# Kernel tuning notes

Measured on AMD Instinct MI355X. Metric: run time of the kernel, lower is better.

## Reference

```python
import jax, jax.numpy as jnp
import numpy as np

B, N, T, H = 16, 512, 100, 64

def setup_inputs() -> dict:
    key = jax.random.key(0)
    ks = jax.random.split(key, 9)
    s = 0.1
    return {
        "x": jax.random.normal(ks[0], (B, N, T), dtype=jnp.float32),
        "conv1_w": jax.random.normal(ks[1], (16, 1, 3), dtype=jnp.float32) * s,
        "conv1_b": jax.random.normal(ks[2], (16,), dtype=jnp.float32) * s,
        "conv2_w": jax.random.normal(ks[3], (32, 16, 3), dtype=jnp.float32) * s,
        "conv2_b": jax.random.normal(ks[4], (32,), dtype=jnp.float32) * s,
        "W_ih": jax.random.normal(ks[5], (3 * H, 32), dtype=jnp.float32) * s,
        "W_hh": jax.random.normal(ks[6], (3 * H, H), dtype=jnp.float32) * s,
        "b_ih": jax.random.normal(ks[7], (3 * H,), dtype=jnp.float32) * s,
        "b_hh": jax.random.normal(ks[8], (3 * H,), dtype=jnp.float32) * s,
    }

def _causal_conv_relu(h, w, b):
    # h: [BN, C_in, T]; left-pad (k-1)*dilation = 2 for causality
    y = jax.lax.conv_general_dilated(
        h, w, window_strides=(1,), padding=[(2, 0)],
        dimension_numbers=("NCH", "OIH", "NCH"))
    return jax.nn.relu(y + b[None, :, None])

def reference(x, conv1_w, conv1_b, conv2_w, conv2_b, W_ih, W_hh, b_ih, b_hh):
    b_, n_, t_ = x.shape
    h = x.reshape(b_ * n_, 1, t_)
    h = _causal_conv_relu(h, conv1_w, conv1_b)   # [BN, 16, T]
    h = _causal_conv_relu(h, conv2_w, conv2_b)   # [BN, 32, T]
    seq = h.transpose(0, 2, 1)                   # [BN, T, 32]
    # precompute input-to-gate projections for all timesteps: [BN, T, 3H]
    xp = jnp.einsum("btc,gc->btg", seq, W_ih) + b_ih
    hdim = W_hh.shape[1]

    def step(hprev, xt):
        gh = hprev @ W_hh.T + b_hh               # [BN, 3H]
        xr, xz, xn = jnp.split(xt, 3, axis=-1)
        hr, hz, hn = jnp.split(gh, 3, axis=-1)
        r = jax.nn.sigmoid(xr + hr)
        z = jax.nn.sigmoid(xz + hz)
        nn_ = jnp.tanh(xn + r * hn)
        hnew = (1.0 - z) * nn_ + z * hprev
        return hnew, None

    h0 = jnp.zeros((b_ * n_, hdim), dtype=x.dtype)
    hf, _ = jax.lax.scan(step, h0, xp.transpose(1, 0, 2))  # scan over T
    return hf.reshape(b_, n_, hdim)
```

## Files before the change

kernel.cpp:

```cpp
#include <hip/hip_runtime.h>
#include <stdint.h>

typedef __attribute__((ext_vector_type(8))) short s16x8;
typedef __attribute__((ext_vector_type(4))) float f32x4;

__device__ __forceinline__ short f2bf(float f){
  union { float f; uint32_t u; } v; v.f = f;
  uint32_t u = v.u;
  u += 0x7fffu + ((u >> 16) & 1u);
  return (short)(u >> 16);
}
__device__ __forceinline__ float sigm_fast(float x){
  float e = __builtin_amdgcn_exp2f(x * -1.44269504f);
  return __builtin_amdgcn_rcpf(1.f + e);
}
__device__ __forceinline__ float tanh_fast(float x){
  float e = __builtin_amdgcn_exp2f(x * 2.88539008f);
  return __builtin_fmaf(-2.f, __builtin_amdgcn_rcpf(e + 1.f), 1.f);
}

#define MFMA16(a, b, c) __builtin_amdgcn_mfma_f32_16x16x32_bf16((a), (b), (c), 0, 0, 0)

__global__ __launch_bounds__(256, 2) void te_fused(
    const float* __restrict__ x,
    const float* __restrict__ w1, const float* __restrict__ b1,
    const float* __restrict__ w2, const float* __restrict__ b2,
    const float* __restrict__ Wih, const float* __restrict__ Whh,
    const float* __restrict__ bih, const float* __restrict__ bhh,
    float* __restrict__ out)
{
  constexpr int T = 100;
  constexpr int M = 16;
  __shared__ float x_s[M * T];
  __shared__ short hA[2][16 * 72];
  __shared__ short ring[4][16 * 24];
  __shared__ short s_s[2][16 * 40];

  const int tid  = threadIdx.x;
  const int lane = tid & 63;
  const int wv   = tid >> 6;
  const int l15  = lane & 15;
  const int lg   = lane >> 4;
  const int seq0 = blockIdx.x * M;

  {
    const float4* gx = reinterpret_cast<const float4*>(x + (size_t)seq0 * T);
    float4* sx = reinterpret_cast<float4*>(x_s);
    for (int i = tid; i < (M * T) / 4; i += 256) sx[i] = gx[i];
  }
  {
    int* p = reinterpret_cast<int*>(&hA[0][0]);
    for (int i = tid; i < (16 * 72) / 2; i += 256) p[i] = 0;
    int* q = reinterpret_cast<int*>(&ring[0][0]);
    for (int i = tid; i < (4 * 16 * 24) / 2; i += 256) q[i] = 0;
  }

  s16x8 WhhHi[3][2], WihHi[3];
  f32x4 bias_r, bias_z, bias_xn, bias_hn;
#pragma unroll
  for (int g = 0; g < 3; ++g) {
    const int n = 64 * g + 16 * wv + l15;
#pragma unroll
    for (int ks = 0; ks < 2; ++ks) {
      const float* p = Whh + n * 64 + ks * 32 + lg * 8;
#pragma unroll
      for (int j = 0; j < 8; ++j) WhhHi[g][ks][j] = f2bf(p[j]);
    }
    const float* q = Wih + n * 32 + lg * 8;
#pragma unroll
    for (int j = 0; j < 8; ++j) WihHi[g][j] = f2bf(q[j]);
    float bi = bih[n], bh = bhh[n];
    if (g == 0) { float v = bi + bh; bias_r  = (f32x4){v, v, v, v}; }
    if (g == 1) { float v = bi + bh; bias_z  = (f32x4){v, v, v, v}; }
    if (g == 2) { bias_xn = (f32x4){bi, bi, bi, bi};
                  bias_hn = (f32x4){bh, bh, bh, bh}; }
  }

  s16x8 cW2[2];
  f32x4 b2v4;
  {
    const int ch = 16 * (wv & 1) + l15;
    float bv = b2[ch];
    b2v4 = (f32x4){bv, bv, bv, bv};
#pragma unroll
    for (int ks = 0; ks < 2; ++ks) {
      s16x8 h8;
#pragma unroll
      for (int j = 0; j < 8; ++j) {
        const int k = ks * 32 + lg * 8 + j;
        const int g = k >> 4, ii = k & 15;
        h8[j] = (g < 3) ? f2bf(w2[ch * 48 + ii * 3 + g]) : (short)0;
      }
      cW2[ks] = h8;
    }
  }

  const int cidx = tid & 127;
  const int csl  = cidx >> 4;
  const int cch  = cidx & 15;
  const float w1v0 = w1[cch * 3 + 0], w1v1 = w1[cch * 3 + 1], w1v2 = w1[cch * 3 + 2];
  const float b1v = b1[cch];

  const int i0a = (lg & 1) * 8;
  const int grp = lg >> 1;
  const short* ringRdBase = &ring[0][0] + l15 * 24 + i0a;
  int sA0off[4], sA1off[4];
#pragma unroll
  for (int p = 0; p < 4; ++p) {
    sA0off[p] = ((p + 3 + grp) & 3) * 384;
    sA1off[p] = ((p + 1 + grp) & 3) * 384;
  }
  const short* sRdBase = &s_s[0][0] + l15 * 40 + lg * 8;
  const short* hRdBase = &hA[0][0] + l15 * 72 + lg * 8;
  short* hWrBase = &hA[0][0] + (lg * 4) * 72 + 16 * wv + l15;
  short* swWr    = &s_s[0][0] + (lg * 4) * 40 + (wv & 1) * 16 + l15;
  short* ringWrA = &ring[0][0] + csl * 24 + cch;
  short* ringWrB = &ring[0][0] + (csl + 8) * 24 + cch;
  const float* xpA = &x_s[csl * T];
  const float* xpB = &x_s[(csl + 8) * T];

  __syncthreads();

#define CONV2_STEP(P_, WB_) do {                                              \
    s16x8 a0 = *reinterpret_cast<const s16x8*>(ringRdBase + sA0off[(P_)]);    \
    s16x8 a1 = *reinterpret_cast<const s16x8*>(ringRdBase + sA1off[(P_)]);    \
    f32x4 sa = MFMA16(a1, cW2[1], MFMA16(a0, cW2[0], b2v4));                  \
    float m0 = sa[0] > 0.f ? sa[0] : 0.f;                                     \
    float m1 = sa[1] > 0.f ? sa[1] : 0.f;                                     \
    float m2 = sa[2] > 0.f ? sa[2] : 0.f;                                     \
    float m3 = sa[3] > 0.f ? sa[3] : 0.f;                                     \
    uint32_t u01, u23;                                                        \
    asm("v_cvt_pk_bf16_f32 %0, %1, %2" : "=v"(u01) : "v"(m0), "v"(m1));       \
    asm("v_cvt_pk_bf16_f32 %0, %1, %2" : "=v"(u23) : "v"(m2), "v"(m3));       \
    swWr[(WB_) * 640 +   0] = (short)(u01 & 0xffff);                          \
    swWr[(WB_) * 640 +  40] = (short)(u01 >> 16);                             \
    swWr[(WB_) * 640 +  80] = (short)(u23 & 0xffff);                          \
    swWr[(WB_) * 640 + 120] = (short)(u23 >> 16);                             \
  } while (0)

  float xaA = 0.f, xbA = 0.f, xaB = 0.f, xbB = 0.f;
  if (wv >= 2) {
    xaA = xpA[0]; xbA = xpA[1];
    xaB = xpB[0]; xbB = xpB[1];
    float cA = b1v + w1v2 * xaA; cA = cA > 0.f ? cA : 0.f;
    float cB = b1v + w1v2 * xaB; cB = cB > 0.f ? cB : 0.f;
    uint32_t cu;
    asm("v_cvt_pk_bf16_f32 %0, %1, %2" : "=v"(cu) : "v"(cA), "v"(cB));
    ringWrA[0] = (short)(cu & 0xffff);
    ringWrB[0] = (short)(cu >> 16);
  }
  __syncthreads();
  if (wv < 2) CONV2_STEP(3, 0);
  if (wv >= 2) {
    float cA = b1v + w1v1 * xaA + w1v2 * xbA; cA = cA > 0.f ? cA : 0.f;
    float cB = b1v + w1v1 * xaB + w1v2 * xbB; cB = cB > 0.f ? cB : 0.f;
    uint32_t cu;
    asm("v_cvt_pk_bf16_f32 %0, %1, %2" : "=v"(cu) : "v"(cA), "v"(cB));
    ringWrA[384] = (short)(cu & 0xffff);
    ringWrB[384] = (short)(cu >> 16);
  }
  __syncthreads();

  float hreg[4] = {0.f, 0.f, 0.f, 0.f};

#define GRU_STEP(T_, P_, C2_, C1_) do {                                       \
    const int rb_ = (P_) & 1, wb_ = rb_ ^ 1;                                  \
    s16x8 as_ = *reinterpret_cast<const s16x8*>(sRdBase + rb_ * 640);         \
    s16x8 ah0 = *reinterpret_cast<const s16x8*>(hRdBase + rb_ * 1152);        \
    s16x8 ah1 = *reinterpret_cast<const s16x8*>(hRdBase + rb_ * 1152 + 32);   \
    __builtin_amdgcn_s_setprio(1);                                            \
    f32x4 pre_r = MFMA16(as_, WihHi[0],                                       \
                  MFMA16(ah1, WhhHi[0][1],                                    \
                  MFMA16(ah0, WhhHi[0][0], bias_r)));                         \
    f32x4 pre_z = MFMA16(as_, WihHi[1],                                       \
                  MFMA16(ah1, WhhHi[1][1],                                    \
                  MFMA16(ah0, WhhHi[1][0], bias_z)));                         \
    f32x4 xn = MFMA16(as_, WihHi[2], bias_xn);                                \
    f32x4 hn = MFMA16(ah1, WhhHi[2][1],                                       \
               MFMA16(ah0, WhhHi[2][0], bias_hn));                            \
    __builtin_amdgcn_s_setprio(0);                                            \
    if ((C2_) && wv < 2) { CONV2_STEP((P_), wb_); }                           \
    if ((C1_) && wv >= 2) {                                                   \
      float xcA = xpA[(T_) + 2], xcB = xpB[(T_) + 2];                         \
      float cA = b1v + w1v0 * xaA + w1v1 * xbA + w1v2 * xcA;                  \
      cA = cA > 0.f ? cA : 0.f;                                               \
      float cB = b1v + w1v0 * xaB + w1v1 * xbB + w1v2 * xcB;                  \
      cB = cB > 0.f ? cB : 0.f;                                               \
      uint32_t cu_;                                                           \
      asm("v_cvt_pk_bf16_f32 %0, %1, %2" : "=v"(cu_) : "v"(cA), "v"(cB));     \
      ringWrA[(((P_) + 2) & 3) * 384] = (short)(cu_ & 0xffff);                \
      ringWrB[(((P_) + 2) & 3) * 384] = (short)(cu_ >> 16);                   \
      xaA = xbA; xbA = xcA; xaB = xbB; xbB = xcB;                             \
    }                                                                         \
    float hnew[4];                                                            \
    _Pragma("unroll")                                                         \
    for (int i2 = 0; i2 < 4; ++i2) {                                          \
      float r = sigm_fast(pre_r[i2]);                                         \
      float z = sigm_fast(pre_z[i2]);                                         \
      float arg = __builtin_fmaf(r, hn[i2], xn[i2]);                          \
      float tn = tanh_fast(arg);                                              \
      float h = __builtin_fmaf(z, hreg[i2] - tn, tn);                         \
      hreg[i2] = h;                                                           \
      hnew[i2] = h;                                                           \
    }                                                                         \
    uint32_t p01, p23;                                                        \
    asm("v_cvt_pk_bf16_f32 %0, %1, %2" : "=v"(p01) : "v"(hnew[0]), "v"(hnew[1])); \
    asm("v_cvt_pk_bf16_f32 %0, %1, %2" : "=v"(p23) : "v"(hnew[2]), "v"(hnew[3])); \
    hWrBase[wb_ * 1152 +   0] = (short)(p01 & 0xffff);                        \
    hWrBase[wb_ * 1152 +  72] = (short)(p01 >> 16);                           \
    hWrBase[wb_ * 1152 + 144] = (short)(p23 & 0xffff);                        \
    hWrBase[wb_ * 1152 + 216] = (short)(p23 >> 16);                           \
    __syncthreads();                                                          \
  } while (0)

#pragma unroll 1
  for (int t = 0; t < 96; t += 4) {
    GRU_STEP(t + 0, 0, true, true);
    GRU_STEP(t + 1, 1, true, true);
    GRU_STEP(t + 2, 2, true, true);
    GRU_STEP(t + 3, 3, true, true);
  }
  GRU_STEP(96, 0, true, true);
  GRU_STEP(97, 1, true, true);
  GRU_STEP(98, 2, true, false);
  GRU_STEP(99, 3, false, false);

#pragma unroll
  for (int i2 = 0; i2 < 4; ++i2) {
    out[(size_t)(seq0 + lg * 4 + i2) * 64 + 16 * wv + l15] = hreg[i2];
  }
}

extern "C" void kernel_launch(void* const* d_in, const int* in_sizes, int n_in,
                              void* d_out, int out_size, void* d_ws, size_t ws_size,
                              hipStream_t stream)
{
  (void)in_sizes; (void)n_in; (void)d_ws; (void)ws_size; (void)out_size;
  const float* x   = (const float*)d_in[0];
  const float* w1  = (const float*)d_in[1];
  const float* b1  = (const float*)d_in[2];
  const float* w2  = (const float*)d_in[3];
  const float* b2  = (const float*)d_in[4];
  const float* Wih = (const float*)d_in[5];
  const float* Whh = (const float*)d_in[6];
  const float* bih = (const float*)d_in[7];
  const float* bhh = (const float*)d_in[8];
  float* out = (float*)d_out;
  te_fused<<<512, 256, 0, stream>>>(x, w1, b1, w2, b2, Wih, Whh, bih, bhh, out);
}
```

Measured before the change: 74.11 us.

## Process two interleaved 16-sequence GRU chains per block and halve the grid

Each block now handles 32 sequences as two independent 16-row GRU chains, interleaved inside every wave, and the grid drops from 512 to 256 blocks. The MFMA work of the two chains is issued together for instruction-level parallelism, and one barrier per timestep now serves both chains. The conv1 and conv2 producer work is spread across all four waves instead of being split by wave role. Launch bounds drop to one block per CU, which frees registers for the doubled state. The s_setprio hints are removed. This gives up the latency hiding that came from two co-resident blocks per CU, and it raises register and LDS use.

```diff
diff --git a/kernel.cpp b/kernel.cpp
--- a/kernel.cpp
+++ b/kernel.cpp
@@ -21,7 +21,7 @@
 
 #define MFMA16(a, b, c) __builtin_amdgcn_mfma_f32_16x16x32_bf16((a), (b), (c), 0, 0, 0)
 
-__global__ __launch_bounds__(256, 2) void te_fused(
+__global__ __launch_bounds__(256, 1) void te_fused(
     const float* __restrict__ x,
     const float* __restrict__ w1, const float* __restrict__ b1,
     const float* __restrict__ w2, const float* __restrict__ b2,
@@ -30,29 +30,30 @@
     float* __restrict__ out)
 {
   constexpr int T = 100;
-  constexpr int M = 16;
-  __shared__ float x_s[M * T];
-  __shared__ short hA[2][16 * 72];
-  __shared__ short ring[4][16 * 24];
-  __shared__ short s_s[2][16 * 40];
+  __shared__ float x_s[32 * T];
+  __shared__ short hA[2][2][16 * 72];
+  __shared__ short ring[2][4][16 * 24];
+  __shared__ short s_s[2][2][16 * 40];
 
   const int tid  = threadIdx.x;
   const int lane = tid & 63;
   const int wv   = tid >> 6;
   const int l15  = lane & 15;
   const int lg   = lane >> 4;
-  const int seq0 = blockIdx.x * M;
+  const int seq0 = blockIdx.x * 32;
 
   {
     const float4* gx = reinterpret_cast<const float4*>(x + (size_t)seq0 * T);
     float4* sx = reinterpret_cast<float4*>(x_s);
-    for (int i = tid; i < (M * T) / 4; i += 256) sx[i] = gx[i];
-  }
-  {
-    int* p = reinterpret_cast<int*>(&hA[0][0]);
+    for (int i = tid; i < (32 * T) / 4; i += 256) sx[i] = gx[i];
+  }
+  {
+    int* p = reinterpret_cast<int*>(&hA[0][0][0]);
     for (int i = tid; i < (16 * 72) / 2; i += 256) p[i] = 0;
-    int* q = reinterpret_cast<int*>(&ring[0][0]);
-    for (int i = tid; i < (4 * 16 * 24) / 2; i += 256) q[i] = 0;
+    int* p1 = reinterpret_cast<int*>(&hA[1][0][0]);
+    for (int i = tid; i < (16 * 72) / 2; i += 256) p1[i] = 0;
+    int* q = reinterpret_cast<int*>(&ring[0][0][0]);
+    for (int i = tid; i < (2 * 4 * 16 * 24) / 2; i += 256) q[i] = 0;
   }
 
   s16x8 WhhHi[3][2], WihHi[3];
@@ -76,10 +77,12 @@
                   bias_hn = (f32x4){bh, bh, bh, bh}; }
   }
 
+  const int cq  = wv >> 1;
+  const int cnt = wv & 1;
   s16x8 cW2[2];
   f32x4 b2v4;
   {
-    const int ch = 16 * (wv & 1) + l15;
+    const int ch = 16 * cnt + l15;
     float bv = b2[ch];
     b2v4 = (f32x4){bv, bv, bv, bv};
 #pragma unroll
@@ -95,35 +98,37 @@
     }
   }
 
-  const int cidx = tid & 127;
-  const int csl  = cidx >> 4;
-  const int cch  = cidx & 15;
-  const float w1v0 = w1[cch * 3 + 0], w1v1 = w1[cch * 3 + 1], w1v2 = w1[cch * 3 + 2];
-  const float b1v = b1[cch];
+  const int sl  = tid >> 4;
+  const int chc = tid & 15;
+  const float w1v0 = w1[chc * 3 + 0], w1v1 = w1[chc * 3 + 1], w1v2 = w1[chc * 3 + 2];
+  const float b1v = b1[chc];
 
   const int i0a = (lg & 1) * 8;
   const int grp = lg >> 1;
-  const short* ringRdBase = &ring[0][0] + l15 * 24 + i0a;
+  const short* ringRdC = &ring[cq][0][0] + l15 * 24 + i0a;
   int sA0off[4], sA1off[4];
 #pragma unroll
   for (int p = 0; p < 4; ++p) {
     sA0off[p] = ((p + 3 + grp) & 3) * 384;
     sA1off[p] = ((p + 1 + grp) & 3) * 384;
   }
-  const short* sRdBase = &s_s[0][0] + l15 * 40 + lg * 8;
-  const short* hRdBase = &hA[0][0] + l15 * 72 + lg * 8;
-  short* hWrBase = &hA[0][0] + (lg * 4) * 72 + 16 * wv + l15;
-  short* swWr    = &s_s[0][0] + (lg * 4) * 40 + (wv & 1) * 16 + l15;
-  short* ringWrA = &ring[0][0] + csl * 24 + cch;
-  short* ringWrB = &ring[0][0] + (csl + 8) * 24 + cch;
-  const float* xpA = &x_s[csl * T];
-  const float* xpB = &x_s[(csl + 8) * T];
+  const short* sRd0 = &s_s[0][0][0] + l15 * 40 + lg * 8;
+  const short* sRd1 = &s_s[1][0][0] + l15 * 40 + lg * 8;
+  const short* hRd0 = &hA[0][0][0] + l15 * 72 + lg * 8;
+  const short* hRd1 = &hA[1][0][0] + l15 * 72 + lg * 8;
+  short* hWr0 = &hA[0][0][0] + (lg * 4) * 72 + 16 * wv + l15;
+  short* hWr1 = &hA[1][0][0] + (lg * 4) * 72 + 16 * wv + l15;
+  short* swWr = &s_s[cq][0][0] + (lg * 4) * 40 + cnt * 16 + l15;
+  short* rwA  = &ring[0][0][0] + sl * 24 + chc;
+  short* rwB  = &ring[1][0][0] + sl * 24 + chc;
+  const float* xpA = &x_s[sl * T];
+  const float* xpB = &x_s[(sl + 16) * T];
 
   __syncthreads();
 
 #define CONV2_STEP(P_, WB_) do {                                              \
-    s16x8 a0 = *reinterpret_cast<const s16x8*>(ringRdBase + sA0off[(P_)]);    \
-    s16x8 a1 = *reinterpret_cast<const s16x8*>(ringRdBase + sA1off[(P_)]);    \
+    s16x8 a0 = *reinterpret_cast<const s16x8*>(ringRdC + sA0off[(P_)]);       \
+    s16x8 a1 = *reinterpret_cast<const s16x8*>(ringRdC + sA1off[(P_)]);       \
     f32x4 sa = MFMA16(a1, cW2[1], MFMA16(a0, cW2[0], b2v4));                  \
     float m0 = sa[0] > 0.f ? sa[0] : 0.f;                                     \
     float m1 = sa[1] > 0.f ? sa[1] : 0.f;                                     \
@@ -138,49 +143,59 @@
     swWr[(WB_) * 640 + 120] = (short)(u23 >> 16);                             \
   } while (0)
 
-  float xaA = 0.f, xbA = 0.f, xaB = 0.f, xbB = 0.f;
-  if (wv >= 2) {
-    xaA = xpA[0]; xbA = xpA[1];
-    xaB = xpB[0]; xbB = xpB[1];
+  float xaA = xpA[0], xbA = xpA[1];
+  float xaB = xpB[0], xbB = xpB[1];
+  {
     float cA = b1v + w1v2 * xaA; cA = cA > 0.f ? cA : 0.f;
     float cB = b1v + w1v2 * xaB; cB = cB > 0.f ? cB : 0.f;
     uint32_t cu;
     asm("v_cvt_pk_bf16_f32 %0, %1, %2" : "=v"(cu) : "v"(cA), "v"(cB));
-    ringWrA[0] = (short)(cu & 0xffff);
-    ringWrB[0] = (short)(cu >> 16);
+    rwA[0] = (short)(cu & 0xffff);
+    rwB[0] = (short)(cu >> 16);
   }
   __syncthreads();
-  if (wv < 2) CONV2_STEP(3, 0);
-  if (wv >= 2) {
+  CONV2_STEP(3, 0);
+  {
     float cA = b1v + w1v1 * xaA + w1v2 * xbA; cA = cA > 0.f ? cA : 0.f;
     float cB = b1v + w1v1 * xaB + w1v2 * xbB; cB = cB > 0.f ? cB : 0.f;
     uint32_t cu;
     asm("v_cvt_pk_bf16_f32 %0, %1, %2" : "=v"(cu) : "v"(cA), "v"(cB));
-    ringWrA[384] = (short)(cu & 0xffff);
-    ringWrB[384] = (short)(cu >> 16);
+    rwA[384] = (short)(cu & 0xffff);
+    rwB[384] = (short)(cu >> 16);
   }
   __syncthreads();
 
-  float hreg[4] = {0.f, 0.f, 0.f, 0.f};
+  float hreg0[4] = {0.f, 0.f, 0.f, 0.f};
+  float hreg1[4] = {0.f, 0.f, 0.f, 0.f};
 
 #define GRU_STEP(T_, P_, C2_, C1_) do {                                       \
     const int rb_ = (P_) & 1, wb_ = rb_ ^ 1;                                  \
-    s16x8 as_ = *reinterpret_cast<const s16x8*>(sRdBase + rb_ * 640);         \
-    s16x8 ah0 = *reinterpret_cast<const s16x8*>(hRdBase + rb_ * 1152);        \
-    s16x8 ah1 = *reinterpret_cast<const s16x8*>(hRdBase + rb_ * 1152 + 32);   \
-    __builtin_amdgcn_s_setprio(1);                                            \
-    f32x4 pre_r = MFMA16(as_, WihHi[0],                                       \
-                  MFMA16(ah1, WhhHi[0][1],                                    \
-                  MFMA16(ah0, WhhHi[0][0], bias_r)));                         \
-    f32x4 pre_z = MFMA16(as_, WihHi[1],                                       \
-                  MFMA16(ah1, WhhHi[1][1],                                    \
-                  MFMA16(ah0, WhhHi[1][0], bias_z)));                         \
-    f32x4 xn = MFMA16(as_, WihHi[2], bias_xn);                                \
-    f32x4 hn = MFMA16(ah1, WhhHi[2][1],                                       \
-               MFMA16(ah0, WhhHi[2][0], bias_hn));                            \
-    __builtin_amdgcn_s_setprio(0);                                            \
-    if ((C2_) && wv < 2) { CONV2_STEP((P_), wb_); }                           \
-    if ((C1_) && wv >= 2) {                                                   \
+    s16x8 as0  = *reinterpret_cast<const s16x8*>(sRd0 + rb_ * 640);           \
+    s16x8 ah00 = *reinterpret_cast<const s16x8*>(hRd0 + rb_ * 1152);          \
+    s16x8 ah01 = *reinterpret_cast<const s16x8*>(hRd0 + rb_ * 1152 + 32);     \
+    s16x8 as1  = *reinterpret_cast<const s16x8*>(sRd1 + rb_ * 640);           \
+    s16x8 ah10 = *reinterpret_cast<const s16x8*>(hRd1 + rb_ * 1152);          \
+    s16x8 ah11 = *reinterpret_cast<const s16x8*>(hRd1 + rb_ * 1152 + 32);     \
+    f32x4 pr0 = MFMA16(as0, WihHi[0],                                         \
+                MFMA16(ah01, WhhHi[0][1],                                     \
+                MFMA16(ah00, WhhHi[0][0], bias_r)));                          \
+    f32x4 pz0 = MFMA16(as0, WihHi[1],                                         \
+                MFMA16(ah01, WhhHi[1][1],                                     \
+                MFMA16(ah00, WhhHi[1][0], bias_z)));                          \
+    f32x4 xn0 = MFMA16(as0, WihHi[2], bias_xn);                               \
+    f32x4 hn0 = MFMA16(ah01, WhhHi[2][1],                                     \
+                MFMA16(ah00, WhhHi[2][0], bias_hn));                          \
+    f32x4 pr1 = MFMA16(as1, WihHi[0],                                         \
+                MFMA16(ah11, WhhHi[0][1],                                     \
+                MFMA16(ah10, WhhHi[0][0], bias_r)));                          \
+    f32x4 pz1 = MFMA16(as1, WihHi[1],                                         \
+                MFMA16(ah11, WhhHi[1][1],                                     \
+                MFMA16(ah10, WhhHi[1][0], bias_z)));                          \
+    f32x4 xn1 = MFMA16(as1, WihHi[2], bias_xn);                               \
+    f32x4 hn1 = MFMA16(ah11, WhhHi[2][1],                                     \
+                MFMA16(ah10, WhhHi[2][0], bias_hn));                          \
+    if (C2_) { CONV2_STEP((P_), wb_); }                                       \
+    if (C1_) {                                                                \
       float xcA = xpA[(T_) + 2], xcB = xpB[(T_) + 2];                         \
       float cA = b1v + w1v0 * xaA + w1v1 * xbA + w1v2 * xcA;                  \
       cA = cA > 0.f ? cA : 0.f;                                               \
@@ -188,28 +203,40 @@
       cB = cB > 0.f ? cB : 0.f;                                               \
       uint32_t cu_;                                                           \
       asm("v_cvt_pk_bf16_f32 %0, %1, %2" : "=v"(cu_) : "v"(cA), "v"(cB));     \
-      ringWrA[(((P_) + 2) & 3) * 384] = (short)(cu_ & 0xffff);                \
-      ringWrB[(((P_) + 2) & 3) * 384] = (short)(cu_ >> 16);                   \
+      rwA[(((P_) + 2) & 3) * 384] = (short)(cu_ & 0xffff);                    \
+      rwB[(((P_) + 2) & 3) * 384] = (short)(cu_ >> 16);                       \
       xaA = xbA; xbA = xcA; xaB = xbB; xbB = xcB;                             \
     }                                                                         \
-    float hnew[4];                                                            \
+    float h0n[4], h1n[4];                                                     \
     _Pragma("unroll")                                                         \
     for (int i2 = 0; i2 < 4; ++i2) {                                          \
-      float r = sigm_fast(pre_r[i2]);                                         \
-      float z = sigm_fast(pre_z[i2]);                                         \
-      float arg = __builtin_fmaf(r, hn[i2], xn[i2]);                          \
-      float tn = tanh_fast(arg);                                              \
-      float h = __builtin_fmaf(z, hreg[i2] - tn, tn);                         \
-      hreg[i2] = h;                                                           \
-      hnew[i2] = h;                                                           \
+      float r = sigm_fast(pr0[i2]);                                           \
+      float z = sigm_fast(pz0[i2]);                                           \
+      float tn = tanh_fast(__builtin_fmaf(r, hn0[i2], xn0[i2]));              \
+      float h = __builtin_fmaf(z, hreg0[i2] - tn, tn);                        \
+      hreg0[i2] = h; h0n[i2] = h;                                             \
     }                                                                         \
-    uint32_t p01, p23;                                                        \
-    asm("v_cvt_pk_bf16_f32 %0, %1, %2" : "=v"(p01) : "v"(hnew[0]), "v"(hnew[1])); \
-    asm("v_cvt_pk_bf16_f32 %0, %1, %2" : "=v"(p23) : "v"(hnew[2]), "v"(hnew[3])); \
-    hWrBase[wb_ * 1152 +   0] = (short)(p01 & 0xffff);                        \
-    hWrBase[wb_ * 1152 +  72] = (short)(p01 >> 16);                           \
-    hWrBase[wb_ * 1152 + 144] = (short)(p23 & 0xffff);                        \
-    hWrBase[wb_ * 1152 + 216] = (short)(p23 >> 16);                           \
+    _Pragma("unroll")                                                         \
+    for (int i2 = 0; i2 < 4; ++i2) {                                          \
+      float r = sigm_fast(pr1[i2]);                                           \
+      float z = sigm_fast(pz1[i2]);                                           \
+      float tn = tanh_fast(__builtin_fmaf(r, hn1[i2], xn1[i2]));              \
+      float h = __builtin_fmaf(z, hreg1[i2] - tn, tn);                        \
+      hreg1[i2] = h; h1n[i2] = h;                                             \
+    }                                                                         \
+    uint32_t a01, a23, b01, b23;                                              \
+    asm("v_cvt_pk_bf16_f32 %0, %1, %2" : "=v"(a01) : "v"(h0n[0]), "v"(h0n[1])); \
+    asm("v_cvt_pk_bf16_f32 %0, %1, %2" : "=v"(a23) : "v"(h0n[2]), "v"(h0n[3])); \
+    asm("v_cvt_pk_bf16_f32 %0, %1, %2" : "=v"(b01) : "v"(h1n[0]), "v"(h1n[1])); \
+    asm("v_cvt_pk_bf16_f32 %0, %1, %2" : "=v"(b23) : "v"(h1n[2]), "v"(h1n[3])); \
+    hWr0[wb_ * 1152 +   0] = (short)(a01 & 0xffff);                           \
+    hWr0[wb_ * 1152 +  72] = (short)(a01 >> 16);                              \
+    hWr0[wb_ * 1152 + 144] = (short)(a23 & 0xffff);                           \
+    hWr0[wb_ * 1152 + 216] = (short)(a23 >> 16);                              \
+    hWr1[wb_ * 1152 +   0] = (short)(b01 & 0xffff);                           \
+    hWr1[wb_ * 1152 +  72] = (short)(b01 >> 16);                              \
+    hWr1[wb_ * 1152 + 144] = (short)(b23 & 0xffff);                           \
+    hWr1[wb_ * 1152 + 216] = (short)(b23 >> 16);                              \
     __syncthreads();                                                          \
   } while (0)
 
@@ -227,7 +254,8 @@
 
 #pragma unroll
   for (int i2 = 0; i2 < 4; ++i2) {
-    out[(size_t)(seq0 + lg * 4 + i2) * 64 + 16 * wv + l15] = hreg[i2];
+    out[(size_t)(seq0 + lg * 4 + i2) * 64 + 16 * wv + l15] = hreg0[i2];
+    out[(size_t)(seq0 + 16 + lg * 4 + i2) * 64 + 16 * wv + l15] = hreg1[i2];
   }
 }
 
@@ -246,5 +274,5 @@
   const float* bih = (const float*)d_in[7];
   const float* bhh = (const float*)d_in[8];
   float* out = (float*)d_out;
-  te_fused<<<512, 256, 0, stream>>>(x, w1, b1, w2, b2, Wih, Whh, bih, bhh, out);
-}
+  te_fused<<<256, 256, 0, stream>>>(x, w1, b1, w2, b2, Wih, Whh, bih, bhh, out);
+}
```

New measurement: 87.51 us. 18.1% more time.
